# Optimization experiments

Hardware: AMD Instinct MI355X
Metric: run time of the kernel (lower is better)

## Reference

```python
import jax, jax.numpy as jnp
import numpy as np

K = 4
TEMPERATURE = 30.0


def setup_inputs() -> dict:
    key = jax.random.key(0)
    ks = jax.random.split(key, 6)
    B, C, H, W_sp = 32, 128, 56, 56
    Cout, kh, kw = 128, 3, 3
    Cred = max(C // 4, 1)
    x = jax.random.normal(ks[0], (B, C, H, W_sp), dtype=jnp.float32)
    # K parallel conv kernels + biases (fan-in scaled init)
    fan = C * kh * kw
    W = jax.random.normal(ks[1], (K, Cout, C, kh, kw), dtype=jnp.float32) / np.sqrt(fan)
    b = jax.random.normal(ks[2], (K, Cout), dtype=jnp.float32) * 0.01
    # attention branch: 1x1 convs == dense on pooled features
    aw1 = jax.random.normal(ks[3], (Cred, C), dtype=jnp.float32) / np.sqrt(C)
    aw2 = jax.random.normal(ks[4], (K, Cred), dtype=jnp.float32) / np.sqrt(Cred)
    return {"x": x, "W": W, "b": b, "aw1": aw1, "aw2": aw2}


def reference(x, W, b, aw1, aw2):
    # attention: global avg pool -> 1x1 conv (dense) -> relu -> 1x1 conv -> softmax(logits/T)
    pooled = jnp.mean(x, axis=(2, 3))                       # [B, C]
    h1 = jax.nn.relu(jnp.einsum('bc,rc->br', pooled, aw1))  # [B, Cred]
    logits = jnp.einsum('br,kr->bk', h1, aw2)               # [B, K]
    attn = jax.nn.softmax(logits / TEMPERATURE, axis=1)     # [B, K]

    pad = 1
    out = None
    for i in range(K):  # fixed small K, structurally distinct kernels
        yi = jax.lax.conv_general_dilated(
            x, W[i], window_strides=(1, 1), padding=[(pad, pad), (pad, pad)],
            dimension_numbers=('NCHW', 'OIHW', 'NCHW'))
        yi = yi + b[i][None, :, None, None]
        yi = yi * attn[:, i][:, None, None, None]
        out = yi if out is None else out + yi
    return out
```

## Files before the change

kernel.cpp:

```cpp
#include <hip/hip_runtime.h>
#include <hip/hip_bf16.h>
#include <stdint.h>

typedef __bf16 bf16x8 __attribute__((ext_vector_type(8)));
typedef float  f32x4  __attribute__((ext_vector_type(4)));
typedef unsigned short u16x8 __attribute__((ext_vector_type(8)));

#define NB 32
#define NC 128
#define NH 56
#define NW 56
#define NK 4
#define NCO 128
#define NCR 32
#define NHW 3136
#define TEMPER 30.0f

#define WS_ATTN   0u
#define WS_BC     4096u
#define WS_ROWSUM 65536u
#define WS_WC     1048576u
#define WS_XT     10485760u

__global__ void xt_kernel(const float* __restrict__ x, __hip_bfloat16* __restrict__ xt,
                          float* __restrict__ rowsum) {
  __shared__ float lds[58 * 133];
  int xcd = blockIdx.x & 7;
  int j   = blockIdx.x >> 3;
  int b   = xcd * 4 + j / 58;
  int hp  = j % 58;
  int blk = b * 58 + hp;
  int h = hp - 1;
  bool hin = (h >= 0) && (h < NH);
  int tid = threadIdx.x;
  if (hin) {
    const float* xrow = x + ((size_t)b * NC) * NHW + (size_t)h * NW;
    for (int i = tid; i < 128 * 14; i += 256) {
      int c = i / 14;
      int w4 = (i - c * 14) * 4;
      float4 v = *(const float4*)(xrow + (size_t)c * NHW + w4);
      int base = (w4 + 1) * 133 + c;
      lds[base]         = v.x;
      lds[base + 133]   = v.y;
      lds[base + 2*133] = v.z;
      lds[base + 3*133] = v.w;
    }
  }
  __syncthreads();
  __hip_bfloat16* orow = xt + (size_t)blk * (58 * 128);
  for (int i = tid; i < 58 * 16; i += 256) {
    int wp = i >> 4;
    int cg = (i & 15) << 3;
    u16x8 o;
    if (!hin || wp == 0 || wp == 57) {
      o = (u16x8)0;
    } else {
      const float* src = lds + wp * 133 + cg;
      #pragma unroll
      for (int jx = 0; jx < 8; ++jx) {
        union { __hip_bfloat16 b; unsigned short u; } cv;
        cv.b = __float2bfloat16(src[jx]);
        o[jx] = cv.u;
      }
    }
    *(u16x8*)(orow + wp * 128 + cg) = o;
  }
  if (hin && tid < 128) {
    float s = 0.f;
    #pragma unroll 8
    for (int wp = 1; wp <= 56; ++wp) s += lds[wp * 133 + tid];
    rowsum[(size_t)blk * 128 + tid] = s;
  }
}

__global__ void attn_kernel(const float* __restrict__ rowsum, const float* __restrict__ aw1,
                            const float* __restrict__ aw2, const float* __restrict__ bias,
                            float* __restrict__ attn, float* __restrict__ bc_out) {
  int b = blockIdx.x;
  __shared__ float sp[NC], h1[NCR], at[NK];
  int t = threadIdx.x;
  if (t < NC) {
    float s = 0.f;
    for (int hp = 1; hp <= 56; ++hp) s += rowsum[((size_t)b * 58 + hp) * 128 + t];
    sp[t] = s * (1.0f / (float)NHW);
  }
  __syncthreads();
  if (t < NCR) {
    float s = 0.f;
    for (int c = 0; c < NC; ++c) s += aw1[t*NC + c] * sp[c];
    h1[t] = s > 0.f ? s : 0.f;
  }
  __syncthreads();
  if (t == 0) {
    float lg[NK], mx = -1e30f;
    for (int k = 0; k < NK; ++k) {
      float s = 0.f;
      for (int r = 0; r < NCR; ++r) s += aw2[k*NCR + r] * h1[r];
      lg[k] = s * (1.0f/TEMPER);
      mx = fmaxf(mx, lg[k]);
    }
    float den = 0.f, e[NK];
    for (int k = 0; k < NK; ++k) { e[k] = expf(lg[k]-mx); den += e[k]; }
    float inv = 1.0f/den;
    for (int k = 0; k < NK; ++k) { at[k] = e[k]*inv; attn[b*NK+k] = at[k]; }
  }
  __syncthreads();
  if (t < NCO) {
    float s = 0.f;
    for (int k = 0; k < NK; ++k) s += at[k] * bias[k*NCO + t];
    bc_out[b*NCO + t] = s;
  }
}

__global__ void combine_kernel(const float* __restrict__ W, const float* __restrict__ attn,
                               __hip_bfloat16* __restrict__ wc) {
  int gid = blockIdx.x;
  int bg  = gid >> 6;
  int tcell = (gid & 63) * 256 + threadIdx.x;
  int co = tcell >> 7, ci = tcell & 127;
  float w[4][9];
  const float* wp = W + ((size_t)co * 128 + ci) * 9;
  #pragma unroll
  for (int k = 0; k < 4; ++k)
    #pragma unroll
    for (int j = 0; j < 9; ++j)
      w[k][j] = wp[(size_t)k * 147456 + j];
  for (int b = bg * 8; b < bg * 8 + 8; ++b) {
    float a0 = attn[b*4+0], a1 = attn[b*4+1], a2 = attn[b*4+2], a3 = attn[b*4+3];
    #pragma unroll
    for (int j = 0; j < 9; ++j) {
      float v = a0*w[0][j] + a1*w[1][j] + a2*w[2][j] + a3*w[3][j];
      wc[(((size_t)b*9 + j) * 128 + co) * 128 + ci] = __float2bfloat16(v);
    }
  }
}

#define RS 2368
#define CS 40
#define BUF4 (4*RS)

#define GLOAD16(src, dst) \
  __builtin_amdgcn_global_load_lds( \
    (const __attribute__((address_space(1))) unsigned int*)(src), \
    (__attribute__((address_space(3))) unsigned int*)(dst), 16, 0, 0)

__global__ __launch_bounds__(256, 4) void conv_kernel(
    const unsigned short* __restrict__ xt,
    const unsigned short* __restrict__ wc,
    const float* __restrict__ bc,
    float* __restrict__ out) {
  __shared__ __align__(16) unsigned short lds_x[2*BUF4];
  const int tid  = threadIdx.x;
  const int lane = tid & 63;
  const int wv   = tid >> 6;
  const int bid = blockIdx.x;
  const int xcd = bid & 7;
  const int jj  = bid >> 3;
  const int b   = xcd * 4 + (jj / 28);
  const int r0  = (jj % 28) * 2;
  const int li = lane & 15;
  const int kg = lane >> 4;

  int srcoff[5];
  #pragma unroll
  for (int i = 0; i < 5; ++i) {
    int q = i*256 + tid;
    int r = q / 296;
    int sl = q - r*296;
    int col = sl / 5;
    int part = sl - col*5;
    if (q < 1184 && col < 58 && part < 4)
      srcoff[i] = ((r0 + r)*58 + col)*128 + part*8;
    else
      srcoff[i] = -1;
  }

  int xoff[7];
  #pragma unroll
  for (int f = 0; f < 7; ++f) {
    int pos = f*16 + li;
    int rB = pos / 56;
    int cB = pos - rB*56;
    xoff[f] = rB*RS + cB*CS + kg*8;
  }
  const f32x4 vzero = {0.f, 0.f, 0.f, 0.f};
  f32x4 acc[2][7];
  #pragma unroll
  for (int mo = 0; mo < 2; ++mo)
    #pragma unroll
    for (int f = 0; f < 7; ++f) acc[mo][f] = vzero;

  const unsigned short* xtg = xt + (size_t)b*(58*58*128);
  const unsigned short* wcA = wc + (size_t)b*(9*128*128) + (wv*32 + li)*128 + kg*8;

  #define STAGE(bufidx, cc) do { \
    unsigned short* dbase = lds_x + (bufidx)*BUF4; \
    _Pragma("unroll") \
    for (int i = 0; i < 5; ++i) { \
      if (srcoff[i] >= 0) \
        GLOAD16(xtg + srcoff[i] + (cc)*32, dbase + i*2048 + wv*512); \
    } \
  } while (0)

  STAGE(0, 0);
  __syncthreads();

  for (int cc = 0; cc < 4; ++cc) {
    if (cc < 3) STAGE((cc + 1) & 1, cc + 1);
    const unsigned short* bx = lds_x + (cc & 1)*BUF4;
    #pragma unroll
    for (int khw = 0; khw < 9; ++khw) {
      const int kh = khw / 3;
      const int kw = khw - kh*3;
      const int koff = kh*RS + kw*CS;
      bf16x8 af[2];
      #pragma unroll
      for (int mo = 0; mo < 2; ++mo)
        af[mo] = *(const bf16x8*)(wcA + khw*16384 + mo*2048 + cc*32);
      bf16x8 bfr[7];
      #pragma unroll
      for (int f = 0; f < 7; ++f)
        bfr[f] = *(const bf16x8*)(bx + xoff[f] + koff);
      __builtin_amdgcn_s_setprio(1);
      #pragma unroll
      for (int mo = 0; mo < 2; ++mo)
        #pragma unroll
        for (int f = 0; f < 7; ++f)
          acc[mo][f] = __builtin_amdgcn_mfma_f32_16x16x32_bf16(af[mo], bfr[f], acc[mo][f], 0, 0, 0);
      __builtin_amdgcn_s_setprio(0);
    }
    __syncthreads();
  }

  float* ob = out + (size_t)b*NCO*NHW;
  #pragma unroll
  for (int mo = 0; mo < 2; ++mo) {
    #pragma unroll
    for (int rg = 0; rg < 4; ++rg) {
      const int co = wv*32 + mo*16 + kg*4 + rg;
      const float bv = bc[b*NCO + co];
      float* orow = ob + (size_t)co*NHW;
      #pragma unroll
      for (int f = 0; f < 7; ++f) {
        int pos = f*16 + li;
        int rB = pos / 56;
        int cB = pos - rB*56;
        orow[(r0 + rB)*56 + cB] = acc[mo][f][rg] + bv;
      }
    }
  }
}

extern "C" void kernel_launch(void* const* d_in, const int* in_sizes, int n_in,
                              void* d_out, int out_size, void* d_ws, size_t ws_size,
                              hipStream_t stream) {
  const float* x   = (const float*)d_in[0];
  const float* W   = (const float*)d_in[1];
  const float* bia = (const float*)d_in[2];
  const float* aw1 = (const float*)d_in[3];
  const float* aw2 = (const float*)d_in[4];
  float* out = (float*)d_out;
  char* ws = (char*)d_ws;
  float* attn   = (float*)(ws + WS_ATTN);
  float* bcm    = (float*)(ws + WS_BC);
  float* rowsum = (float*)(ws + WS_ROWSUM);
  __hip_bfloat16* wc = (__hip_bfloat16*)(ws + WS_WC);
  __hip_bfloat16* xt = (__hip_bfloat16*)(ws + WS_XT);

  xt_kernel<<<NB*58, 256, 0, stream>>>(x, xt, rowsum);
  attn_kernel<<<NB, 128, 0, stream>>>(rowsum, aw1, aw2, bia, attn, bcm);
  combine_kernel<<<256, 256, 0, stream>>>(W, attn, wc);
  conv_kernel<<<896, 256, 0, stream>>>((const unsigned short*)xt,
                                       (const unsigned short*)wc, bcm, out);
}
```

Before: 77.19 us.

## Enlarge conv tile to 8 rows with LDS-staged weights and 512-thread blocks

The conv kernel now computes an 8-row by 128-channel output tile per 512-thread block: 8 waves are split 2x4 over output channels and pixels, and each wave accumulates 4x7 MFMA tiles. Per-batch combined weights are staged through LDS (via registers) each channel chunk, so they are read from global once per block rather than by every wave. This is meant to raise arithmetic intensity and cut redundant global weight and halo traffic. In exchange it drops the double-buffered prefetch, adds two barriers per chunk, raises accumulator register pressure, uses much more LDS, and launches only 224 blocks, which risks poor occupancy and latency hiding.

```diff
diff --git a/kernel.cpp b/kernel.cpp
--- a/kernel.cpp
+++ b/kernel.cpp
@@ -5,6 +5,7 @@
 typedef __bf16 bf16x8 __attribute__((ext_vector_type(8)));
 typedef float  f32x4  __attribute__((ext_vector_type(4)));
 typedef unsigned short u16x8 __attribute__((ext_vector_type(8)));
+typedef unsigned int   u32x4 __attribute__((ext_vector_type(4)));
 
 #define NB 32
 #define NC 128
@@ -137,112 +138,127 @@
 
 #define RS 2368
 #define CS 40
-#define BUF4 (4*RS)
+#define AKS 5120
 
 #define GLOAD16(src, dst) \
   __builtin_amdgcn_global_load_lds( \
     (const __attribute__((address_space(1))) unsigned int*)(src), \
     (__attribute__((address_space(3))) unsigned int*)(dst), 16, 0, 0)
 
-__global__ __launch_bounds__(256, 4) void conv_kernel(
+__global__ __launch_bounds__(512, 2) void conv_kernel(
     const unsigned short* __restrict__ xt,
     const unsigned short* __restrict__ wc,
     const float* __restrict__ bc,
     float* __restrict__ out) {
-  __shared__ __align__(16) unsigned short lds_x[2*BUF4];
+  __shared__ __align__(16) unsigned short lds_a[9*AKS];
+  __shared__ __align__(16) unsigned short lds_b[10*RS];
   const int tid  = threadIdx.x;
   const int lane = tid & 63;
   const int wv   = tid >> 6;
-  const int bid = blockIdx.x;
-  const int xcd = bid & 7;
-  const int jj  = bid >> 3;
-  const int b   = xcd * 4 + (jj / 28);
-  const int r0  = (jj % 28) * 2;
-  const int li = lane & 15;
-  const int kg = lane >> 4;
-
-  int srcoff[5];
-  #pragma unroll
-  for (int i = 0; i < 5; ++i) {
-    int q = i*256 + tid;
+  const int wm   = wv >> 2;
+  const int wn   = wv & 3;
+  const int bid  = blockIdx.x;
+  const int xcd  = bid & 7;
+  const int jj   = bid >> 3;
+  const int b    = xcd*4 + jj/7;
+  const int r0   = (jj % 7) * 8;
+  const int li   = lane & 15;
+  const int kg   = lane >> 4;
+
+  int srcB[6];
+  #pragma unroll
+  for (int i = 0; i < 6; ++i) {
+    int q = i*512 + tid;
     int r = q / 296;
     int sl = q - r*296;
     int col = sl / 5;
     int part = sl - col*5;
-    if (q < 1184 && col < 58 && part < 4)
-      srcoff[i] = ((r0 + r)*58 + col)*128 + part*8;
-    else
-      srcoff[i] = -1;
+    srcB[i] = (q < 2960 && col < 58 && part < 4)
+              ? ((r0 + r)*58 + col)*128 + part*8 : -1;
+  }
+  int aS[9], aD[9];
+  #pragma unroll
+  for (int i = 0; i < 9; ++i) {
+    int s = i*512 + tid;
+    int khw = s >> 9;
+    int co  = (s & 511) >> 2;
+    int part = s & 3;
+    aS[i] = (khw*128 + co)*128 + part*8;
+    aD[i] = (khw*128 + co)*40 + part*8;
   }
 
   int xoff[7];
   #pragma unroll
   for (int f = 0; f < 7; ++f) {
-    int pos = f*16 + li;
+    int pos = wn*112 + f*16 + li;
     int rB = pos / 56;
     int cB = pos - rB*56;
     xoff[f] = rB*RS + cB*CS + kg*8;
   }
+  const int aRead = (wm*64 + li)*40 + kg*8;
+
   const f32x4 vzero = {0.f, 0.f, 0.f, 0.f};
-  f32x4 acc[2][7];
-  #pragma unroll
-  for (int mo = 0; mo < 2; ++mo)
+  f32x4 acc[4][7];
+  #pragma unroll
+  for (int mo = 0; mo < 4; ++mo)
     #pragma unroll
     for (int f = 0; f < 7; ++f) acc[mo][f] = vzero;
 
   const unsigned short* xtg = xt + (size_t)b*(58*58*128);
-  const unsigned short* wcA = wc + (size_t)b*(9*128*128) + (wv*32 + li)*128 + kg*8;
-
-  #define STAGE(bufidx, cc) do { \
-    unsigned short* dbase = lds_x + (bufidx)*BUF4; \
-    _Pragma("unroll") \
-    for (int i = 0; i < 5; ++i) { \
-      if (srcoff[i] >= 0) \
-        GLOAD16(xtg + srcoff[i] + (cc)*32, dbase + i*2048 + wv*512); \
-    } \
-  } while (0)
-
-  STAGE(0, 0);
-  __syncthreads();
+  const unsigned short* wcg = wc + (size_t)b*(9*128*128);
 
   for (int cc = 0; cc < 4; ++cc) {
-    if (cc < 3) STAGE((cc + 1) & 1, cc + 1);
-    const unsigned short* bx = lds_x + (cc & 1)*BUF4;
+    u32x4 areg[9];
+    #pragma unroll
+    for (int i = 0; i < 9; ++i)
+      areg[i] = *(const u32x4*)(wcg + aS[i] + cc*32);
+
+    __syncthreads();
+
+    #pragma unroll
+    for (int i = 0; i < 6; ++i)
+      if (srcB[i] >= 0)
+        GLOAD16(xtg + srcB[i] + cc*32, lds_b + (i*512 + wv*64)*8);
+    #pragma unroll
+    for (int i = 0; i < 9; ++i)
+      *(u32x4*)(lds_a + aD[i]) = areg[i];
+
+    __syncthreads();
+
     #pragma unroll
     for (int khw = 0; khw < 9; ++khw) {
       const int kh = khw / 3;
       const int kw = khw - kh*3;
+      bf16x8 af[4];
+      #pragma unroll
+      for (int mo = 0; mo < 4; ++mo)
+        af[mo] = *(const bf16x8*)(lds_a + khw*AKS + aRead + mo*640);
       const int koff = kh*RS + kw*CS;
-      bf16x8 af[2];
-      #pragma unroll
-      for (int mo = 0; mo < 2; ++mo)
-        af[mo] = *(const bf16x8*)(wcA + khw*16384 + mo*2048 + cc*32);
       bf16x8 bfr[7];
       #pragma unroll
       for (int f = 0; f < 7; ++f)
-        bfr[f] = *(const bf16x8*)(bx + xoff[f] + koff);
+        bfr[f] = *(const bf16x8*)(lds_b + xoff[f] + koff);
       __builtin_amdgcn_s_setprio(1);
       #pragma unroll
-      for (int mo = 0; mo < 2; ++mo)
+      for (int mo = 0; mo < 4; ++mo)
         #pragma unroll
         for (int f = 0; f < 7; ++f)
           acc[mo][f] = __builtin_amdgcn_mfma_f32_16x16x32_bf16(af[mo], bfr[f], acc[mo][f], 0, 0, 0);
       __builtin_amdgcn_s_setprio(0);
     }
-    __syncthreads();
   }
 
   float* ob = out + (size_t)b*NCO*NHW;
   #pragma unroll
-  for (int mo = 0; mo < 2; ++mo) {
+  for (int mo = 0; mo < 4; ++mo) {
     #pragma unroll
     for (int rg = 0; rg < 4; ++rg) {
-      const int co = wv*32 + mo*16 + kg*4 + rg;
+      const int co = wm*64 + mo*16 + kg*4 + rg;
       const float bv = bc[b*NCO + co];
       float* orow = ob + (size_t)co*NHW;
       #pragma unroll
       for (int f = 0; f < 7; ++f) {
-        int pos = f*16 + li;
+        int pos = wn*112 + f*16 + li;
         int rB = pos / 56;
         int cB = pos - rB*56;
         orow[(r0 + rB)*56 + cB] = acc[mo][f][rg] + bv;
@@ -270,6 +286,6 @@
   xt_kernel<<<NB*58, 256, 0, stream>>>(x, xt, rowsum);
   attn_kernel<<<NB, 128, 0, stream>>>(rowsum, aw1, aw2, bia, attn, bcm);
   combine_kernel<<<256, 256, 0, stream>>>(W, attn, wc);
-  conv_kernel<<<896, 256, 0, stream>>>((const unsigned short*)xt,
+  conv_kernel<<<224, 512, 0, stream>>>((const unsigned short*)xt,
                                        (const unsigned short*)wc, bcm, out);
 }
```

Result: faster. 66.41 us (-14.0%).

## Stage conv weights through LDS per kernel row, drop x double-buffering

Applied to the files above, without the earlier changes.

The conv kernel now stages the combined weight tile into LDS with global_load_lds for each kernel row, rather than having every wave read the weights straight from global memory. The input tile is single-buffered and reloaded once per channel chunk. Out-of-range staging lanes are clamped instead of skipped. The aim is to cut redundant global weight traffic and latency, at the cost of losing the overlap of loads with compute, adding more __syncthreads barriers, and lowering launch_bounds occupancy from 4 to 3.

```diff
diff --git a/kernel.cpp b/kernel.cpp
--- a/kernel.cpp
+++ b/kernel.cpp
@@ -137,31 +137,33 @@
 
 #define RS 2368
 #define CS 40
-#define BUF4 (4*RS)
+#define BCHP 1280
+#define ACH 1536
 
 #define GLOAD16(src, dst) \
   __builtin_amdgcn_global_load_lds( \
     (const __attribute__((address_space(1))) unsigned int*)(src), \
     (__attribute__((address_space(3))) unsigned int*)(dst), 16, 0, 0)
 
-__global__ __launch_bounds__(256, 4) void conv_kernel(
+__global__ __launch_bounds__(256, 3) void conv_kernel(
     const unsigned short* __restrict__ xt,
     const unsigned short* __restrict__ wc,
     const float* __restrict__ bc,
     float* __restrict__ out) {
-  __shared__ __align__(16) unsigned short lds_x[2*BUF4];
+  __shared__ __align__(16) unsigned short lds_b[BCHP*8];
+  __shared__ __align__(16) unsigned short lds_a[ACH*8];
   const int tid  = threadIdx.x;
   const int lane = tid & 63;
-  const int wv   = tid >> 6;
-  const int bid = blockIdx.x;
-  const int xcd = bid & 7;
-  const int jj  = bid >> 3;
-  const int b   = xcd * 4 + (jj / 28);
-  const int r0  = (jj % 28) * 2;
-  const int li = lane & 15;
-  const int kg = lane >> 4;
-
-  int srcoff[5];
+  const int wm   = tid >> 6;
+  const int bid  = blockIdx.x;
+  const int xcd  = bid & 7;
+  const int jj   = bid >> 3;
+  const int b    = xcd*4 + jj/28;
+  const int r0   = (jj % 28) * 2;
+  const int li   = lane & 15;
+  const int kg   = lane >> 4;
+
+  int srcB[5];
   #pragma unroll
   for (int i = 0; i < 5; ++i) {
     int q = i*256 + tid;
@@ -169,10 +171,19 @@
     int sl = q - r*296;
     int col = sl / 5;
     int part = sl - col*5;
-    if (q < 1184 && col < 58 && part < 4)
-      srcoff[i] = ((r0 + r)*58 + col)*128 + part*8;
-    else
-      srcoff[i] = -1;
+    int rc = r > 3 ? 3 : r;
+    int cl = col > 57 ? 57 : col;
+    int pc = part > 3 ? 3 : part;
+    srcB[i] = ((r0 + rc)*58 + cl)*128 + pc*8;
+  }
+  int srcA[6];
+  #pragma unroll
+  for (int i = 0; i < 6; ++i) {
+    int c = i*256 + tid;
+    int khwL = c >> 9;
+    int co   = (c & 511) >> 2;
+    int part = c & 3;
+    srcA[i] = (khwL*128 + co)*128 + part*8;
   }
 
   int xoff[7];
@@ -183,6 +194,8 @@
     int cB = pos - rB*56;
     xoff[f] = rB*RS + cB*CS + kg*8;
   }
+  const int aRead = (wm*32 + li)*32 + kg*8;
+
   const f32x4 vzero = {0.f, 0.f, 0.f, 0.f};
   f32x4 acc[2][7];
   #pragma unroll
@@ -191,45 +204,38 @@
     for (int f = 0; f < 7; ++f) acc[mo][f] = vzero;
 
   const unsigned short* xtg = xt + (size_t)b*(58*58*128);
-  const unsigned short* wcA = wc + (size_t)b*(9*128*128) + (wv*32 + li)*128 + kg*8;
-
-  #define STAGE(bufidx, cc) do { \
-    unsigned short* dbase = lds_x + (bufidx)*BUF4; \
-    _Pragma("unroll") \
-    for (int i = 0; i < 5; ++i) { \
-      if (srcoff[i] >= 0) \
-        GLOAD16(xtg + srcoff[i] + (cc)*32, dbase + i*2048 + wv*512); \
-    } \
-  } while (0)
-
-  STAGE(0, 0);
-  __syncthreads();
+  const unsigned short* wcg = wc + (size_t)b*(9*128*128);
 
   for (int cc = 0; cc < 4; ++cc) {
-    if (cc < 3) STAGE((cc + 1) & 1, cc + 1);
-    const unsigned short* bx = lds_x + (cc & 1)*BUF4;
-    #pragma unroll
-    for (int khw = 0; khw < 9; ++khw) {
-      const int kh = khw / 3;
-      const int kw = khw - kh*3;
-      const int koff = kh*RS + kw*CS;
-      bf16x8 af[2];
-      #pragma unroll
-      for (int mo = 0; mo < 2; ++mo)
-        af[mo] = *(const bf16x8*)(wcA + khw*16384 + mo*2048 + cc*32);
-      bf16x8 bfr[7];
-      #pragma unroll
-      for (int f = 0; f < 7; ++f)
-        bfr[f] = *(const bf16x8*)(bx + xoff[f] + koff);
-      __builtin_amdgcn_s_setprio(1);
-      #pragma unroll
-      for (int mo = 0; mo < 2; ++mo)
+    #pragma unroll
+    for (int kh = 0; kh < 3; ++kh) {
+      __syncthreads();
+      #pragma unroll
+      for (int i = 0; i < 6; ++i)
+        GLOAD16(wcg + kh*49152 + srcA[i] + cc*32, lds_a + (i*256 + wm*64)*8);
+      if (kh == 0) {
+        #pragma unroll
+        for (int i = 0; i < 5; ++i)
+          GLOAD16(xtg + srcB[i] + cc*32, lds_b + (i*256 + wm*64)*8);
+      }
+      __syncthreads();
+      #pragma unroll
+      for (int kwl = 0; kwl < 3; ++kwl) {
+        bf16x8 af[2];
+        #pragma unroll
+        for (int mo = 0; mo < 2; ++mo)
+          af[mo] = *(const bf16x8*)(lds_a + kwl*4096 + aRead + mo*512);
+        bf16x8 bfr[7];
         #pragma unroll
         for (int f = 0; f < 7; ++f)
-          acc[mo][f] = __builtin_amdgcn_mfma_f32_16x16x32_bf16(af[mo], bfr[f], acc[mo][f], 0, 0, 0);
-      __builtin_amdgcn_s_setprio(0);
-    }
-    __syncthreads();
+          bfr[f] = *(const bf16x8*)(lds_b + xoff[f] + kh*RS + kwl*CS);
+        #pragma unroll
+        for (int mo = 0; mo < 2; ++mo)
+          #pragma unroll
+          for (int f = 0; f < 7; ++f)
+            acc[mo][f] = __builtin_amdgcn_mfma_f32_16x16x32_bf16(af[mo], bfr[f], acc[mo][f], 0, 0, 0);
+      }
+    }
   }
 
   float* ob = out + (size_t)b*NCO*NHW;
@@ -237,7 +243,7 @@
   for (int mo = 0; mo < 2; ++mo) {
     #pragma unroll
     for (int rg = 0; rg < 4; ++rg) {
-      const int co = wv*32 + mo*16 + kg*4 + rg;
+      const int co = wm*32 + mo*16 + kg*4 + rg;
       const float bv = bc[b*NCO + co];
       float* orow = ob + (size_t)co*NHW;
       #pragma unroll
```

Result: faster. 71.57 us (-7.3%).
